# Kernel optimization log

Hardware: AMD Instinct MI355X
Metric: run time of the kernel (lower is better)

## Reference

```python
import jax, jax.numpy as jnp
import numpy as np

B, S, D = 2, 2048, 4096
H, KVH, HD = 32, 8, 128
REPEATS = H // KVH
SCALE = HD ** -0.5


def setup_inputs() -> dict:
    key = jax.random.key(0)
    ks = jax.random.split(key, 5)
    x = jax.random.normal(ks[0], (B, S, D), dtype=jnp.float32)
    # RoPE tables: shape (S, HD//2)
    t = jnp.arange(S, dtype=jnp.float32)
    inv_freq = 1.0 / (10000.0 ** (jnp.arange(0, HD, 2, dtype=jnp.float32) / HD))
    freqs = jnp.outer(t, inv_freq)
    freqs_cos = jnp.cos(freqs)
    freqs_sin = jnp.sin(freqs)
    # causal additive mask [B, S, S]
    i = jnp.arange(S)
    causal = jnp.where(i[:, None] >= i[None, :], 0.0, -1e9).astype(jnp.float32)
    mask = jnp.broadcast_to(causal[None], (B, S, S))
    positions = jnp.arange(S, dtype=jnp.int32)
    w_std = 0.02
    wq = jax.random.normal(ks[1], (D, H * HD), dtype=jnp.float32) * w_std
    wk = jax.random.normal(ks[2], (D, KVH * HD), dtype=jnp.float32) * w_std
    wv = jax.random.normal(ks[3], (D, KVH * HD), dtype=jnp.float32) * w_std
    wo = jax.random.normal(ks[4], (H * HD, D), dtype=jnp.float32) * w_std
    return dict(x=x, freqs_cos=freqs_cos, freqs_sin=freqs_sin, mask=mask,
                wq=wq, wk=wk, wv=wv, wo=wo, positions=positions)


def _apply_rope(t, fc, fs):
    # t: [B, S, h, HD]; interleaved (real, imag) pairs along last dim
    tr = t.reshape(t.shape[:-1] + (HD // 2, 2))
    r, i = tr[..., 0], tr[..., 1]
    c = fc[None, :, None, :]  # [1, S, 1, HD//2]
    s = fs[None, :, None, :]
    out_r = r * c - i * s
    out_i = r * s + i * c
    return jnp.stack([out_r, out_i], axis=-1).reshape(t.shape)


def reference(x, freqs_cos, freqs_sin, mask, wq, wk, wv, wo, positions):
    bsz, seqlen, _ = x.shape
    xq = (x @ wq).reshape(bsz, seqlen, H, HD)
    xk = (x @ wk).reshape(bsz, seqlen, KVH, HD)
    xv = (x @ wv).reshape(bsz, seqlen, KVH, HD)
    xq = _apply_rope(xq, freqs_cos, freqs_sin)
    xk = _apply_rope(xk, freqs_cos, freqs_sin)
    # GQA: repeat_interleave over kv-head dim
    key = jnp.repeat(xk, REPEATS, axis=2)   # [B, S, H, HD]
    value = jnp.repeat(xv, REPEATS, axis=2)
    q = xq.transpose(0, 2, 1, 3)            # [B, H, S, HD]
    k = key.transpose(0, 2, 1, 3)
    v = value.transpose(0, 2, 1, 3)
    scores = jnp.einsum('bhqd,bhkd->bhqk', q, k) * SCALE
    scores = scores + mask[:, None, :, :]
    probs = jax.nn.softmax(scores.astype(jnp.float32), axis=-1)
    out = jnp.einsum('bhqk,bhkd->bhqd', probs, v)
    out = out.transpose(0, 2, 1, 3).reshape(bsz, seqlen, H * HD)
    out = jnp.nan_to_num(out)
    return out @ wo
```

## Files before the change

### kernel.cpp

```cpp
#include <hip/hip_runtime.h>

typedef unsigned short ushort_t;
typedef unsigned int uint32;

#define SCALE_F 0.08838834764831845f

using bf16x8 = __attribute__((ext_vector_type(8))) short;
using f32x4  = __attribute__((ext_vector_type(4))) float;
using u32x4  = __attribute__((ext_vector_type(4))) uint32;
using u32x2  = __attribute__((ext_vector_type(2))) uint32;

__device__ __forceinline__ float b2f(ushort_t h) {
  union { uint32 u; float f; } v; v.u = ((uint32)h) << 16; return v.f;
}
__device__ __forceinline__ ushort_t f2b(float f) {
  union { float f; uint32 u; } v; v.f = f;
  uint32 r = (v.u + 0x7fffu + ((v.u >> 16) & 1u)) >> 16;
  return (ushort_t)r;
}
__device__ __forceinline__ uint32 pk2(float a, float b) {
  union { float f; uint32 u; } x, y; x.f = a; y.f = b;
  return __builtin_amdgcn_perm(y.u + 0x8000u, x.u + 0x8000u, 0x07060302u);
}
__device__ __forceinline__ void gl2lds16(const void* g, void* l) {
  __builtin_amdgcn_global_load_lds(
      (const __attribute__((address_space(1))) uint32*)g,
      (__attribute__((address_space(3))) uint32*)l, 16, 0, 0);
}

constexpr int LDP = 40;


__global__ __launch_bounds__(256)
void xconv(const float* __restrict__ x, ushort_t* __restrict__ xb) {
  size_t i = ((size_t)blockIdx.x * 256 + threadIdx.x) * 8;
  f32x4 a = *(const f32x4*)&x[i];
  f32x4 b = *(const f32x4*)&x[i + 4];
  u32x4 p = {pk2(a[0], a[1]), pk2(a[2], a[3]), pk2(b[0], b[1]), pk2(b[2], b[3])};
  *(u32x4*)&xb[i] = p;
}

__global__ __launch_bounds__(256)
void wtrans(const float* __restrict__ src, ushort_t* __restrict__ dst, int N) {
  __shared__ float ts[32][33];
  int n0 = blockIdx.x * 32, k0 = blockIdx.y * 32;
  int tid = threadIdx.x;
  {
    int r = tid >> 3, c4 = (tid & 7) * 4;
    f32x4 v = *(const f32x4*)&src[(size_t)(k0 + r) * N + n0 + c4];
    ts[r][c4 + 0] = v[0]; ts[r][c4 + 1] = v[1];
    ts[r][c4 + 2] = v[2]; ts[r][c4 + 3] = v[3];
  }
  __syncthreads();
  int rn = tid >> 3, ck = (tid & 7) * 4;
  u32x2 p = {pk2(ts[ck + 0][rn], ts[ck + 1][rn]),
             pk2(ts[ck + 2][rn], ts[ck + 3][rn])};
  *(u32x2*)&dst[(size_t)(n0 + rn) * 4096 + k0 + ck] = p;
}

template <int AMODE>
__device__ __forceinline__ void gemm_core_bf(const ushort_t* __restrict__ A,
                                             const ushort_t* __restrict__ B,
                                             int m0, int n0, ushort_t* As,
                                             ushort_t* Bs, f32x4 acc[4][4]) {
  const int K = 4096;
  int tid = threadIdx.x;
  int lane = tid & 63, w = tid >> 6, q = lane >> 4, cl = lane & 15;
  int wr = (w >> 1) * 64, wc = (w & 1) * 64;
  int wub = (tid & 192) * 8;
  for (int k0 = 0; k0 < K; k0 += 32) {
    __syncthreads();
#pragma unroll
    for (int i = 0; i < 2; ++i) {
      int slot = i * 256 + tid;
      int r = slot >> 2, c = slot & 3;
      const ushort_t* ga;
      if (AMODE == 0) {
        ga = A + (size_t)(m0 + r) * K + k0 + c * 8;
      } else {
        int m = m0 + r, bb = m >> 11, s = m & 2047;
        int k = k0 + c * 8;
        int hh = k >> 7, dg = (k >> 5) & 3;
        ga = A + ((((size_t)(bb * 32 + hh) * 32 + (s >> 6)) * 4 + dg) * 64 +
                  (s & 63)) * 32 + (k & 31);
      }
      gl2lds16(ga, As + i * 2048 + wub);
      gl2lds16(B + (size_t)(n0 + r) * K + k0 + c * 8, Bs + i * 2048 + wub);
    }
    __syncthreads();
    bf16x8 af[4], bfr[4];
#pragma unroll
    for (int rt = 0; rt < 4; ++rt)
      af[rt] = *(const bf16x8*)&As[(wr + rt * 16 + cl) * 32 + q * 8];
#pragma unroll
    for (int ct = 0; ct < 4; ++ct)
      bfr[ct] = *(const bf16x8*)&Bs[(wc + ct * 16 + cl) * 32 + q * 8];
#pragma unroll
    for (int rt = 0; rt < 4; ++rt)
#pragma unroll
      for (int ct = 0; ct < 4; ++ct)
        acc[rt][ct] = __builtin_amdgcn_mfma_f32_16x16x32_bf16(
            af[rt], bfr[ct], acc[rt][ct], 0, 0, 0);
  }
}

__global__ __launch_bounds__(256, 3)
void qkv_gemm(const ushort_t* __restrict__ xb, const ushort_t* __restrict__ wt,
              const float* __restrict__ fc, const float* __restrict__ fs,
              ushort_t* __restrict__ qg, ushort_t* __restrict__ kg,
              ushort_t* __restrict__ vg) {
  __shared__ ushort_t As[128 * 32];
  __shared__ ushort_t Bs[128 * 32];
  int n0 = blockIdx.x * 128, m0 = blockIdx.y * 128;
  f32x4 acc[4][4] = {};
  gemm_core_bf<0>(xb, wt, m0, n0, As, Bs, acc);
  int tid = threadIdx.x;
  int lane = tid & 63, w = tid >> 6, q = lane >> 4, cl = lane & 15;
  int wr = (w >> 1) * 64, wc = (w & 1) * 64;
  if (n0 < 5120) {
    ushort_t* dst = (n0 < 4096) ? qg : kg;
    int NHH = (n0 < 4096) ? 32 : 8;
    int nc = (n0 < 4096) ? n0 : n0 - 4096;
    for (int rt = 0; rt < 4; ++rt)
      for (int ct = 0; ct < 4; ++ct)
        for (int rg = 0; rg < 4; ++rg) {
          int row = m0 + wr + rt * 16 + q * 4 + rg;
          int b = row >> 11, s = row & 2047;
          int col = nc + wc + ct * 16 + cl;
          int hh = col >> 7, d = col & 127;
          float val = acc[rt][ct][rg];
          float par = __shfl_xor(val, 1);
          float cf = fc[(size_t)s * 64 + (d >> 1)];
          float sf = fs[(size_t)s * 64 + (d >> 1)];
          float o = val * cf + par * ((d & 1) ? sf : -sf);
          size_t off =
              ((((size_t)(b * NHH + hh) * 32 + (s >> 6)) * 4 + (d >> 5)) * 64 +
               (s & 63)) * 32 + (d & 31);
          dst[off] = f2b(o);
        }
  } else {
    int nc = n0 - 5120;
    for (int rt = 0; rt < 4; ++rt)
      for (int ct = 0; ct < 4; ++ct)
        for (int rg = 0; rg < 4; ++rg) {
          int row = m0 + wr + rt * 16 + q * 4 + rg;
          int b = row >> 11, s = row & 2047;
          int col = nc + wc + ct * 16 + cl;
          int kvh = col >> 7, d = col & 127;
          size_t off =
              ((((size_t)(b * 8 + kvh) * 32 + (s >> 6)) * 2 + ((s >> 5) & 1)) *
                   128 + d) * 32 + (s & 31);
          vg[off] = f2b(acc[rt][ct][rg]);
        }
  }
}

__global__ __launch_bounds__(256, 3)
void out_gemm(const ushort_t* __restrict__ attn,
              const ushort_t* __restrict__ wot, float* __restrict__ out) {
  __shared__ ushort_t As[128 * 32];
  __shared__ ushort_t Bs[128 * 32];
  int n0 = blockIdx.x * 128, m0 = blockIdx.y * 128;
  f32x4 acc[4][4] = {};
  gemm_core_bf<1>(attn, wot, m0, n0, As, Bs, acc);
  int tid = threadIdx.x;
  int lane = tid & 63, w = tid >> 6, q = lane >> 4, cl = lane & 15;
  int wr = (w >> 1) * 64, wc = (w & 1) * 64;
  for (int rt = 0; rt < 4; ++rt)
    for (int ct = 0; ct < 4; ++ct)
      for (int rg = 0; rg < 4; ++rg) {
        int row = m0 + wr + rt * 16 + q * 4 + rg;
        int col = n0 + wc + ct * 16 + cl;
        out[(size_t)row * 4096 + col] = acc[rt][ct][rg];
      }
}


template <int AMODE>
__device__ __forceinline__ void gemm_core_cvt(const void* __restrict__ A,
                                              const float* __restrict__ B, int K,
                                              int NB, int m0, int nb0,
                                              ushort_t* As, ushort_t* Bs,
                                              f32x4 acc[4][4]) {
  int tid = threadIdx.x;
  int lane = tid & 63, w = tid >> 6, q = lane >> 4, cl = lane & 15;
  int wr = (w >> 1) * 64, wc = (w & 1) * 64;
  int ar = tid >> 1, ah = tid & 1;
  int bn = tid & 127, bh = tid >> 7;
  for (int k0 = 0; k0 < K; k0 += 32) {
    __syncthreads();
    if (AMODE == 0) {
      const float* ap = &((const float*)A)[(size_t)(m0 + ar) * K + k0 + ah * 16];
      f32x4 a0 = *(const f32x4*)(ap + 0);
      f32x4 a1 = *(const f32x4*)(ap + 4);
      f32x4 a2 = *(const f32x4*)(ap + 8);
      f32x4 a3 = *(const f32x4*)(ap + 12);
      u32x4 p0 = {pk2(a0[0], a0[1]), pk2(a0[2], a0[3]), pk2(a1[0], a1[1]),
                  pk2(a1[2], a1[3])};
      u32x4 p1 = {pk2(a2[0], a2[1]), pk2(a2[2], a2[3]), pk2(a3[0], a3[1]),
                  pk2(a3[2], a3[3])};
      *(u32x4*)&As[ar * LDP + ah * 16] = p0;
      *(u32x4*)&As[ar * LDP + ah * 16 + 8] = p1;
    } else {
      int m = m0 + ar, bb = m >> 11, s = m & 2047;
      int k = k0 + ah * 16;
      int hh = k >> 7, dg = (k >> 5) & 3, el = k & 31;
      size_t off =
          ((((size_t)(bb * 32 + hh) * 32 + (s >> 6)) * 4 + dg) * 64 +
           (s & 63)) * 32 + el;
      const ushort_t* ap = (const ushort_t*)A + off;
      u32x4 v0 = *(const u32x4*)(ap + 0);
      u32x4 v1 = *(const u32x4*)(ap + 8);
      *(u32x4*)&As[ar * LDP + ah * 16] = v0;
      *(u32x4*)&As[ar * LDP + ah * 16 + 8] = v1;
    }
    {
      float bv[16];
#pragma unroll
      for (int j = 0; j < 16; ++j)
        bv[j] = B[(size_t)(k0 + bh * 16 + j) * NB + nb0 + bn];
      u32x4 p0 = {pk2(bv[0], bv[1]), pk2(bv[2], bv[3]), pk2(bv[4], bv[5]),
                  pk2(bv[6], bv[7])};
      u32x4 p1 = {pk2(bv[8], bv[9]), pk2(bv[10], bv[11]), pk2(bv[12], bv[13]),
                  pk2(bv[14], bv[15])};
      *(u32x4*)&Bs[bn * LDP + bh * 16] = p0;
      *(u32x4*)&Bs[bn * LDP + bh * 16 + 8] = p1;
    }
    __syncthreads();
    bf16x8 af[4], bfr[4];
    for (int rt = 0; rt < 4; ++rt)
      af[rt] = *(const bf16x8*)&As[(wr + rt * 16 + cl) * LDP + q * 8];
    for (int ct = 0; ct < 4; ++ct)
      bfr[ct] = *(const bf16x8*)&Bs[(wc + ct * 16 + cl) * LDP + q * 8];
    for (int rt = 0; rt < 4; ++rt)
      for (int ct = 0; ct < 4; ++ct)
        acc[rt][ct] = __builtin_amdgcn_mfma_f32_16x16x32_bf16(
            af[rt], bfr[ct], acc[rt][ct], 0, 0, 0);
  }
}

__global__ __launch_bounds__(256, 3)
void qkv_gemm_cvt(const float* __restrict__ x, const float* __restrict__ wq,
                  const float* __restrict__ wk, const float* __restrict__ wv,
                  const float* __restrict__ fc, const float* __restrict__ fs,
                  ushort_t* __restrict__ qg, ushort_t* __restrict__ kg,
                  ushort_t* __restrict__ vg) {
  __shared__ ushort_t As[128 * LDP];
  __shared__ ushort_t Bs[128 * LDP];
  int n0 = blockIdx.x * 128, m0 = blockIdx.y * 128;
  const float* Bp; int NB, nc;
  if (n0 < 4096)      { Bp = wq; NB = 4096; nc = n0; }
  else if (n0 < 5120) { Bp = wk; NB = 1024; nc = n0 - 4096; }
  else                { Bp = wv; NB = 1024; nc = n0 - 5120; }
  f32x4 acc[4][4] = {};
  gemm_core_cvt<0>(x, Bp, 4096, NB, m0, nc, As, Bs, acc);
  int tid = threadIdx.x;
  int lane = tid & 63, w = tid >> 6, q = lane >> 4, cl = lane & 15;
  int wr = (w >> 1) * 64, wc = (w & 1) * 64;
  if (n0 < 5120) {
    ushort_t* dst = (n0 < 4096) ? qg : kg;
    int NHH = (n0 < 4096) ? 32 : 8;
    for (int rt = 0; rt < 4; ++rt)
      for (int ct = 0; ct < 4; ++ct)
        for (int rg = 0; rg < 4; ++rg) {
          int row = m0 + wr + rt * 16 + q * 4 + rg;
          int b = row >> 11, s = row & 2047;
          int col = nc + wc + ct * 16 + cl;
          int hh = col >> 7, d = col & 127;
          float val = acc[rt][ct][rg];
          float par = __shfl_xor(val, 1);
          float cf = fc[(size_t)s * 64 + (d >> 1)];
          float sf = fs[(size_t)s * 64 + (d >> 1)];
          float o = val * cf + par * ((d & 1) ? sf : -sf);
          size_t off =
              ((((size_t)(b * NHH + hh) * 32 + (s >> 6)) * 4 + (d >> 5)) * 64 +
               (s & 63)) * 32 + (d & 31);
          dst[off] = f2b(o);
        }
  } else {
    for (int rt = 0; rt < 4; ++rt)
      for (int ct = 0; ct < 4; ++ct)
        for (int rg = 0; rg < 4; ++rg) {
          int row = m0 + wr + rt * 16 + q * 4 + rg;
          int b = row >> 11, s = row & 2047;
          int col = nc + wc + ct * 16 + cl;
          int kvh = col >> 7, d = col & 127;
          size_t off =
              ((((size_t)(b * 8 + kvh) * 32 + (s >> 6)) * 2 + ((s >> 5) & 1)) *
                   128 + d) * 32 + (s & 31);
          vg[off] = f2b(acc[rt][ct][rg]);
        }
  }
}

__global__ __launch_bounds__(256, 3)
void out_gemm_cvt(const ushort_t* __restrict__ attn,
                  const float* __restrict__ wo, float* __restrict__ out) {
  __shared__ ushort_t As[128 * LDP];
  __shared__ ushort_t Bs[128 * LDP];
  int n0 = blockIdx.x * 128, m0 = blockIdx.y * 128;
  f32x4 acc[4][4] = {};
  gemm_core_cvt<1>(attn, wo, 4096, 4096, m0, n0, As, Bs, acc);
  int tid = threadIdx.x;
  int lane = tid & 63, w = tid >> 6, q = lane >> 4, cl = lane & 15;
  int wr = (w >> 1) * 64, wc = (w & 1) * 64;
  for (int rt = 0; rt < 4; ++rt)
    for (int ct = 0; ct < 4; ++ct)
      for (int rg = 0; rg < 4; ++rg) {
        int row = m0 + wr + rt * 16 + q * 4 + rg;
        int col = n0 + wc + ct * 16 + cl;
        out[(size_t)row * 4096 + col] = acc[rt][ct][rg];
      }
}

__device__ __forceinline__ void stage_tile(const ushort_t* src, ushort_t* dst,
                                           int tid) {
  for (int cc = 0; cc < 4; ++cc)
    gl2lds16(src + (size_t)(cc * 256 + tid) * 8,
             dst + (size_t)(cc * 256 + (tid & 192)) * 8);
}

__global__ __launch_bounds__(256, 2)
void flash_attn(ushort_t* __restrict__ qg, const ushort_t* __restrict__ kg,
                const ushort_t* __restrict__ vg) {
  __shared__ ushort_t Ks[2][8192];
  __shared__ ushort_t Vs[2][8192];
  __shared__ ushort_t Ps[4096];
  int tid = threadIdx.x;
  int w = tid >> 6, lane = tid & 63, q = lane >> 4, cl = lane & 15;
  int idx = blockIdx.x;
  int qb = 31 - (idx >> 6);
  int bh = idx & 63;
  int b = bh >> 5, h = bh & 31, kvh = h >> 2;

  ushort_t* qt = qg + ((size_t)(b * 32 + h) * 32 + qb) * 8192;
  bf16x8 aq[4];
  for (int ks = 0; ks < 4; ++ks)
    aq[ks] = *(const bf16x8*)&qt[ks * 2048 + (w * 16 + cl) * 32 + q * 8];

  const ushort_t* kb = kg + ((size_t)(b * 8 + kvh) * 32) * 8192;
  const ushort_t* vb = vg + ((size_t)(b * 8 + kvh) * 32) * 8192;
  stage_tile(kb, Ks[0], tid);
  stage_tile(vb, Vs[0], tid);

  f32x4 oacc[8] = {};
  float m_i[4], l_i[4];
  for (int rg = 0; rg < 4; ++rg) { m_i[rg] = -3e30f; l_i[rg] = 0.f; }

  for (int jb = 0; jb <= qb; ++jb) {
    __syncthreads();
    int cur = jb & 1, nxt = (jb + 1) & 1;
    int jn = (jb + 1 > qb) ? qb : jb + 1;
    stage_tile(kb + (size_t)jn * 8192, Ks[nxt], tid);
    stage_tile(vb + (size_t)jn * 8192, Vs[nxt], tid);
    f32x4 sacc[4] = {};
    for (int ks = 0; ks < 4; ++ks)
      for (int ct = 0; ct < 4; ++ct) {
        bf16x8 bk =
            *(const bf16x8*)&Ks[cur][ks * 2048 + (ct * 16 + cl) * 32 + q * 8];
        sacc[ct] =
            __builtin_amdgcn_mfma_f32_16x16x32_bf16(aq[ks], bk, sacc[ct], 0, 0, 0);
      }
    float pv[4][4], mt[4];
    bool diag = (jb == qb);
    for (int rg = 0; rg < 4; ++rg) mt[rg] = -3e30f;
    for (int ct = 0; ct < 4; ++ct)
      for (int rg = 0; rg < 4; ++rg) {
        float sv = sacc[ct][rg] * SCALE_F;
        if (diag) {
          int rrow = w * 16 + q * 4 + rg;
          int ccol = ct * 16 + cl;
          if (ccol > rrow) sv = -3e30f;
        }
        pv[ct][rg] = sv;
        mt[rg] = fmaxf(mt[rg], sv);
      }
    for (int off = 1; off < 16; off <<= 1)
      for (int rg = 0; rg < 4; ++rg)
        mt[rg] = fmaxf(mt[rg], __shfl_xor(mt[rg], off));
    float alpha[4], rs[4];
    for (int rg = 0; rg < 4; ++rg) {
      float mn = fmaxf(m_i[rg], mt[rg]);
      alpha[rg] = __expf(m_i[rg] - mn);
      m_i[rg] = mn;
      rs[rg] = 0.f;
    }
    for (int ct = 0; ct < 4; ++ct)
      for (int rg = 0; rg < 4; ++rg) {
        float p = __expf(pv[ct][rg] - m_i[rg]);
        pv[ct][rg] = p;
        rs[rg] += p;
      }
    for (int off = 1; off < 16; off <<= 1)
      for (int rg = 0; rg < 4; ++rg) rs[rg] += __shfl_xor(rs[rg], off);
    for (int rg = 0; rg < 4; ++rg) l_i[rg] = l_i[rg] * alpha[rg] + rs[rg];
    for (int nt = 0; nt < 8; ++nt)
      for (int rg = 0; rg < 4; ++rg) oacc[nt][rg] *= alpha[rg];
    for (int ct = 0; ct < 4; ++ct)
      for (int rg = 0; rg < 4; ++rg) {
        int off_ = w * 1024 + (ct >> 1) * 512 + (q * 4 + rg) * 32 +
                   (ct & 1) * 16 + cl;
        Ps[off_] = f2b(pv[ct][rg]);
      }
    for (int ks2 = 0; ks2 < 2; ++ks2) {
      bf16x8 pa = *(const bf16x8*)&Ps[w * 1024 + ks2 * 512 + cl * 32 + q * 8];
      for (int nt = 0; nt < 8; ++nt) {
        bf16x8 bv =
            *(const bf16x8*)&Vs[cur][ks2 * 4096 + (nt * 16 + cl) * 32 + q * 8];
        oacc[nt] =
            __builtin_amdgcn_mfma_f32_16x16x32_bf16(pa, bv, oacc[nt], 0, 0, 0);
      }
    }
  }
  for (int nt = 0; nt < 8; ++nt)
    for (int rg = 0; rg < 4; ++rg) {
      float v = oacc[nt][rg] / l_i[rg];
      int rowt = w * 16 + q * 4 + rg;
      int d = nt * 16 + cl;
      qt[(d >> 5) * 2048 + rowt * 32 + (d & 31)] = f2b(v);
    }
}

extern "C" void kernel_launch(void* const* d_in, const int* in_sizes, int n_in,
                              void* d_out, int out_size, void* d_ws,
                              size_t ws_size, hipStream_t stream) {
  const float* x  = (const float*)d_in[0];
  const float* fc = (const float*)d_in[1];
  const float* fs = (const float*)d_in[2];
  const float* wq = (const float*)d_in[4];
  const float* wk = (const float*)d_in[5];
  const float* wv = (const float*)d_in[6];
  const float* wo = (const float*)d_in[7];
  ushort_t* ws = (ushort_t*)d_ws;

  ushort_t* qg = ws;
  ushort_t* kg = qg + (size_t)4096 * 4096;
  ushort_t* vg = kg + (size_t)4096 * 1024;

  if (ws_size >= (size_t)128 * 1024 * 1024) {
    ushort_t* wt = vg + (size_t)4096 * 1024;
    ushort_t* xb = wt + (size_t)6144 * 4096;
    xconv<<<8192, 256, 0, stream>>>(x, xb);
    wtrans<<<dim3(128, 128), 256, 0, stream>>>(wq, wt, 4096);
    wtrans<<<dim3(32, 128), 256, 0, stream>>>(wk, wt + (size_t)4096 * 4096, 1024);
    wtrans<<<dim3(32, 128), 256, 0, stream>>>(wv, wt + (size_t)5120 * 4096, 1024);
    qkv_gemm<<<dim3(48, 32), 256, 0, stream>>>(xb, wt, fc, fs, qg, kg, vg);
    wtrans<<<dim3(128, 128), 256, 0, stream>>>(wo, xb, 4096);
    flash_attn<<<2048, 256, 0, stream>>>(qg, kg, vg);
    out_gemm<<<dim3(32, 32), 256, 0, stream>>>(qg, xb, (float*)d_out);
  } else {
    qkv_gemm_cvt<<<dim3(48, 32), 256, 0, stream>>>(x, wq, wk, wv, fc, fs, qg,
                                                   kg, vg);
    flash_attn<<<2048, 256, 0, stream>>>(qg, kg, vg);
    out_gemm_cvt<<<dim3(32, 32), 256, 0, stream>>>(qg, wo, (float*)d_out);
  }
}
```

Baseline: 820.3 us.

## Rewrite QKV and output GEMMs as 8-wave multi-stage pipelined kernels

Replaces the 256-thread 128x128 GEMM cores with 512-thread kernels using larger tiles (128x256 for QKV, 256x256 for output), a 4-deep LDS ring buffer with global_load_lds prefetch issued between MFMA phases, explicit vmcnt waits and barriers, and s_setprio around the MFMA clusters. LDS rows use an XOR swizzle to avoid bank conflicts, and block IDs are remapped so neighbouring blocks share operand tiles in L2. The aim is to hide global-load latency behind matrix work and raise arithmetic intensity. In exchange it uses much more LDS and registers, and the hand-counted vmcnt waits and k-clamping at the tail are fragile.

```diff
diff --git a/kernel.cpp b/kernel.cpp
--- a/kernel.cpp
+++ b/kernel.cpp
@@ -26,6 +26,18 @@
   __builtin_amdgcn_global_load_lds(
       (const __attribute__((address_space(1))) uint32*)g,
       (__attribute__((address_space(3))) uint32*)l, 16, 0, 0);
+}
+__device__ __forceinline__ void fence_mem() { asm volatile("" ::: "memory"); }
+__device__ __forceinline__ void bar() {
+  fence_mem();
+  __builtin_amdgcn_s_barrier();
+  fence_mem();
+}
+template <int N>
+__device__ __forceinline__ void waitvm() {
+  if constexpr (N == 6) asm volatile("s_waitcnt vmcnt(6)" ::: "memory");
+  else if constexpr (N == 8) asm volatile("s_waitcnt vmcnt(8)" ::: "memory");
+  else asm volatile("s_waitcnt vmcnt(0)" ::: "memory");
 }
 
 constexpr int LDP = 40;
@@ -58,77 +70,124 @@
   *(u32x2*)&dst[(size_t)(n0 + rn) * 4096 + k0 + ck] = p;
 }
 
-template <int AMODE>
-__device__ __forceinline__ void gemm_core_bf(const ushort_t* __restrict__ A,
-                                             const ushort_t* __restrict__ B,
-                                             int m0, int n0, ushort_t* As,
-                                             ushort_t* Bs, f32x4 acc[4][4]) {
-  const int K = 4096;
-  int tid = threadIdx.x;
-  int lane = tid & 63, w = tid >> 6, q = lane >> 4, cl = lane & 15;
-  int wr = (w >> 1) * 64, wc = (w & 1) * 64;
-  int wub = (tid & 192) * 8;
-  for (int k0 = 0; k0 < K; k0 += 32) {
-    __syncthreads();
+
+template <int ROWS, int AMODE>
+__device__ __forceinline__ void stage_region(const ushort_t* __restrict__ P,
+                                             int row0, int k, ushort_t* lds,
+                                             int tid) {
 #pragma unroll
-    for (int i = 0; i < 2; ++i) {
-      int slot = i * 256 + tid;
-      int r = slot >> 2, c = slot & 3;
-      const ushort_t* ga;
-      if (AMODE == 0) {
-        ga = A + (size_t)(m0 + r) * K + k0 + c * 8;
-      } else {
-        int m = m0 + r, bb = m >> 11, s = m & 2047;
-        int k = k0 + c * 8;
-        int hh = k >> 7, dg = (k >> 5) & 3;
-        ga = A + ((((size_t)(bb * 32 + hh) * 32 + (s >> 6)) * 4 + dg) * 64 +
-                  (s & 63)) * 32 + (k & 31);
-      }
-      gl2lds16(ga, As + i * 2048 + wub);
-      gl2lds16(B + (size_t)(n0 + r) * K + k0 + c * 8, Bs + i * 2048 + wub);
-    }
-    __syncthreads();
-    bf16x8 af[4], bfr[4];
+  for (int i = 0; i < ROWS / 128; ++i) {
+    int s = i * 512 + tid;
+    int r = s >> 2, c = s & 3;
+    int qq = c ^ ((r >> 1) & 3);
+    const ushort_t* ga;
+    if (AMODE == 0) {
+      ga = P + (size_t)(row0 + r) * 4096 + k + qq * 8;
+    } else {
+      int m = row0 + r, bb = m >> 11, ss = m & 2047;
+      int kk = k + qq * 8;
+      int hh = kk >> 7, dg = (kk >> 5) & 3;
+      ga = P + ((((size_t)(bb * 32 + hh) * 32 + (ss >> 6)) * 4 + dg) * 64 +
+                (ss & 63)) * 32 + (kk & 31);
+    }
+    gl2lds16(ga, lds + ((size_t)(i * 512 + (tid & 448))) * 8);
+  }
+}
+
+template <int BM, int VMC, int AMODE>
+__device__ __forceinline__ void gemm8_core(const ushort_t* __restrict__ A,
+                                           const ushort_t* __restrict__ B,
+                                           int m0, int n0, ushort_t* As,
+                                           ushort_t* Bs, f32x4 (*acc)[4]) {
+  constexpr int FR = BM / 32;
+  constexpr int ASZ = BM * 32;
+  constexpr int BSZ = 256 * 32;
+  const int tid = threadIdx.x;
+  const int lane = tid & 63, q = lane >> 4, cl = lane & 15;
+  const int w = tid >> 6, wrow = w >> 2, wcol = w & 3;
+
+  auto phase = [&](int pl, int qc, auto issue, bool dovm) {
+    bf16x8 af[FR], bfr[2];
+    const ushort_t* ap = As + pl * ASZ;
+    const ushort_t* bp = Bs + pl * BSZ;
 #pragma unroll
-    for (int rt = 0; rt < 4; ++rt)
-      af[rt] = *(const bf16x8*)&As[(wr + rt * 16 + cl) * 32 + q * 8];
+    for (int fr = 0; fr < FR; ++fr) {
+      int rr = wrow * (BM / 2) + fr * 16 + cl;
+      af[fr] = *(const bf16x8*)&ap[rr * 32 + (q ^ ((rr >> 1) & 3)) * 8];
+    }
 #pragma unroll
-    for (int ct = 0; ct < 4; ++ct)
-      bfr[ct] = *(const bf16x8*)&Bs[(wc + ct * 16 + cl) * 32 + q * 8];
+    for (int fb = 0; fb < 2; ++fb) {
+      int rn = wcol * 64 + qc * 32 + fb * 16 + cl;
+      bfr[fb] = *(const bf16x8*)&bp[rn * 32 + (q ^ ((rn >> 1) & 3)) * 8];
+    }
+    issue();
+    bar();
+    __builtin_amdgcn_s_setprio(1);
 #pragma unroll
-    for (int rt = 0; rt < 4; ++rt)
+    for (int fr = 0; fr < FR; ++fr)
 #pragma unroll
-      for (int ct = 0; ct < 4; ++ct)
-        acc[rt][ct] = __builtin_amdgcn_mfma_f32_16x16x32_bf16(
-            af[rt], bfr[ct], acc[rt][ct], 0, 0, 0);
-  }
-}
-
-__global__ __launch_bounds__(256, 3)
-void qkv_gemm(const ushort_t* __restrict__ xb, const ushort_t* __restrict__ wt,
-              const float* __restrict__ fc, const float* __restrict__ fs,
-              ushort_t* __restrict__ qg, ushort_t* __restrict__ kg,
-              ushort_t* __restrict__ vg) {
-  __shared__ ushort_t As[128 * 32];
-  __shared__ ushort_t Bs[128 * 32];
-  int n0 = blockIdx.x * 128, m0 = blockIdx.y * 128;
+      for (int fb = 0; fb < 2; ++fb)
+        acc[fr][qc * 2 + fb] = __builtin_amdgcn_mfma_f32_16x16x32_bf16(
+            af[fr], bfr[fb], acc[fr][qc * 2 + fb], 0, 0, 0);
+    __builtin_amdgcn_s_setprio(0);
+    if (dovm) waitvm<VMC>();
+    bar();
+  };
+
+  stage_region<BM, AMODE>(A, m0, 0, As + 0 * ASZ, tid);
+  stage_region<256, 0>(B, n0, 0, Bs + 0 * BSZ, tid);
+  stage_region<BM, AMODE>(A, m0, 32, As + 1 * ASZ, tid);
+  stage_region<256, 0>(B, n0, 32, Bs + 1 * BSZ, tid);
+  stage_region<BM, AMODE>(A, m0, 64, As + 2 * ASZ, tid);
+  stage_region<256, 0>(B, n0, 64, Bs + 2 * BSZ, tid);
+  waitvm<VMC>();
+  bar();
+
+  for (int it = 0; it < 32; ++it) {
+    int k1h = it * 128 + 96;
+    int t2 = it * 128 + 128; if (t2 > 4032) t2 = 4032;
+    int t3 = it * 128 + 192; if (t3 > 4032) t3 = 4032;
+    phase(0, 0, [&] { stage_region<BM, AMODE>(A, m0, k1h, As + 3 * ASZ, tid); }, false);
+    phase(0, 1, [&] { stage_region<256, 0>(B, n0, k1h, Bs + 3 * BSZ, tid); }, true);
+    phase(1, 0, [&] { stage_region<BM, AMODE>(A, m0, t2, As + 0 * ASZ, tid); }, false);
+    phase(1, 1, [&] { stage_region<256, 0>(B, n0, t2, Bs + 0 * BSZ, tid); }, true);
+    phase(2, 0, [&] { stage_region<BM, AMODE>(A, m0, t2 + 32, As + 1 * ASZ, tid); }, false);
+    phase(2, 1, [&] { stage_region<256, 0>(B, n0, t2 + 32, Bs + 1 * BSZ, tid); }, true);
+    phase(3, 0, [&] { stage_region<BM, AMODE>(A, m0, t3, As + 2 * ASZ, tid); }, false);
+    phase(3, 1, [&] { stage_region<256, 0>(B, n0, t3, Bs + 2 * BSZ, tid); }, true);
+  }
+  waitvm<0>();
+  bar();
+}
+
+__global__ __launch_bounds__(512, 2)
+void qkv_gemm8(const ushort_t* __restrict__ xb, const ushort_t* __restrict__ wt,
+               const float* __restrict__ fc, const float* __restrict__ fs,
+               ushort_t* __restrict__ qg, ushort_t* __restrict__ kg,
+               ushort_t* __restrict__ vg) {
+  __shared__ ushort_t As[4 * 128 * 32];
+  __shared__ ushort_t Bs[4 * 256 * 32];
+  int bid = blockIdx.x;
+  int swz = (bid & 7) * 96 + (bid >> 3);
+  int tx = swz / 32, ty = swz % 32;
+  int n0 = tx * 256, m0 = ty * 128;
   f32x4 acc[4][4] = {};
-  gemm_core_bf<0>(xb, wt, m0, n0, As, Bs, acc);
-  int tid = threadIdx.x;
-  int lane = tid & 63, w = tid >> 6, q = lane >> 4, cl = lane & 15;
-  int wr = (w >> 1) * 64, wc = (w & 1) * 64;
+  gemm8_core<128, 6, 0>(xb, wt, m0, n0, As, Bs, acc);
+  const int tid = threadIdx.x;
+  const int lane = tid & 63, q = lane >> 4, cl = lane & 15;
+  const int w = tid >> 6, wrow = w >> 2, wcol = w & 3;
   if (n0 < 5120) {
     ushort_t* dst = (n0 < 4096) ? qg : kg;
     int NHH = (n0 < 4096) ? 32 : 8;
     int nc = (n0 < 4096) ? n0 : n0 - 4096;
-    for (int rt = 0; rt < 4; ++rt)
-      for (int ct = 0; ct < 4; ++ct)
+    for (int fr = 0; fr < 4; ++fr)
+      for (int fcc = 0; fcc < 4; ++fcc)
         for (int rg = 0; rg < 4; ++rg) {
-          int row = m0 + wr + rt * 16 + q * 4 + rg;
+          int row = m0 + wrow * 64 + fr * 16 + q * 4 + rg;
           int b = row >> 11, s = row & 2047;
-          int col = nc + wc + ct * 16 + cl;
+          int col = nc + wcol * 64 + fcc * 16 + cl;
           int hh = col >> 7, d = col & 127;
-          float val = acc[rt][ct][rg];
+          float val = acc[fr][fcc][rg];
           float par = __shfl_xor(val, 1);
           float cf = fc[(size_t)s * 64 + (d >> 1)];
           float sf = fs[(size_t)s * 64 + (d >> 1)];
@@ -140,38 +199,41 @@
         }
   } else {
     int nc = n0 - 5120;
-    for (int rt = 0; rt < 4; ++rt)
-      for (int ct = 0; ct < 4; ++ct)
+    for (int fr = 0; fr < 4; ++fr)
+      for (int fcc = 0; fcc < 4; ++fcc)
         for (int rg = 0; rg < 4; ++rg) {
-          int row = m0 + wr + rt * 16 + q * 4 + rg;
+          int row = m0 + wrow * 64 + fr * 16 + q * 4 + rg;
           int b = row >> 11, s = row & 2047;
-          int col = nc + wc + ct * 16 + cl;
+          int col = nc + wcol * 64 + fcc * 16 + cl;
           int kvh = col >> 7, d = col & 127;
           size_t off =
               ((((size_t)(b * 8 + kvh) * 32 + (s >> 6)) * 2 + ((s >> 5) & 1)) *
                    128 + d) * 32 + (s & 31);
-          vg[off] = f2b(acc[rt][ct][rg]);
+          vg[off] = f2b(acc[fr][fcc][rg]);
         }
   }
 }
 
-__global__ __launch_bounds__(256, 3)
-void out_gemm(const ushort_t* __restrict__ attn,
-              const ushort_t* __restrict__ wot, float* __restrict__ out) {
-  __shared__ ushort_t As[128 * 32];
-  __shared__ ushort_t Bs[128 * 32];
-  int n0 = blockIdx.x * 128, m0 = blockIdx.y * 128;
-  f32x4 acc[4][4] = {};
-  gemm_core_bf<1>(attn, wot, m0, n0, As, Bs, acc);
-  int tid = threadIdx.x;
-  int lane = tid & 63, w = tid >> 6, q = lane >> 4, cl = lane & 15;
-  int wr = (w >> 1) * 64, wc = (w & 1) * 64;
-  for (int rt = 0; rt < 4; ++rt)
-    for (int ct = 0; ct < 4; ++ct)
+__global__ __launch_bounds__(512, 2)
+void out_gemm8(const ushort_t* __restrict__ attn,
+               const ushort_t* __restrict__ wot, float* __restrict__ out) {
+  __shared__ ushort_t As[4 * 256 * 32];
+  __shared__ ushort_t Bs[4 * 256 * 32];
+  int bid = blockIdx.x;
+  int swz = (bid & 7) * 32 + (bid >> 3);
+  int tx = swz >> 4, ty = swz & 15;
+  int n0 = tx * 256, m0 = ty * 256;
+  f32x4 acc[8][4] = {};
+  gemm8_core<256, 8, 1>(attn, wot, m0, n0, As, Bs, acc);
+  const int tid = threadIdx.x;
+  const int lane = tid & 63, q = lane >> 4, cl = lane & 15;
+  const int w = tid >> 6, wrow = w >> 2, wcol = w & 3;
+  for (int fr = 0; fr < 8; ++fr)
+    for (int fcc = 0; fcc < 4; ++fcc)
       for (int rg = 0; rg < 4; ++rg) {
-        int row = m0 + wr + rt * 16 + q * 4 + rg;
-        int col = n0 + wc + ct * 16 + cl;
-        out[(size_t)row * 4096 + col] = acc[rt][ct][rg];
+        int row = m0 + wrow * 128 + fr * 16 + q * 4 + rg;
+        int col = n0 + wcol * 64 + fcc * 16 + cl;
+        out[(size_t)row * 4096 + col] = acc[fr][fcc][rg];
       }
 }
 
@@ -444,10 +506,10 @@
     wtrans<<<dim3(128, 128), 256, 0, stream>>>(wq, wt, 4096);
     wtrans<<<dim3(32, 128), 256, 0, stream>>>(wk, wt + (size_t)4096 * 4096, 1024);
     wtrans<<<dim3(32, 128), 256, 0, stream>>>(wv, wt + (size_t)5120 * 4096, 1024);
-    qkv_gemm<<<dim3(48, 32), 256, 0, stream>>>(xb, wt, fc, fs, qg, kg, vg);
+    qkv_gemm8<<<768, 512, 0, stream>>>(xb, wt, fc, fs, qg, kg, vg);
     wtrans<<<dim3(128, 128), 256, 0, stream>>>(wo, xb, 4096);
     flash_attn<<<2048, 256, 0, stream>>>(qg, kg, vg);
-    out_gemm<<<dim3(32, 32), 256, 0, stream>>>(qg, xb, (float*)d_out);
+    out_gemm8<<<256, 512, 0, stream>>>(qg, xb, (float*)d_out);
   } else {
     qkv_gemm_cvt<<<dim3(48, 32), 256, 0, stream>>>(x, wq, wk, wv, fc, fs, qg,
                                                    kg, vg);
```

Result: slower. 839.1 us (+2.3%).
